# Kernel tuning notes

Hardware: AMD Instinct MI355X
Metric: run time of the kernel (lower is better)

Reference implementation:

```python
import jax, jax.numpy as jnp
import numpy as np

N = 32768      # total nodes (512 graphs x 64 padded nodes)
E = 262144     # edges (avg degree 8)
F_IN = 74      # atom feature dim
D0 = 128       # dim_embedding
D1 = 256       # hidden feats
B = 512        # batch_size (graphs)
NPG = 64       # nodes per graph
EPS = 1e-5     # BatchNorm1d eps


def setup_inputs() -> dict:
    key = jax.random.key(0)
    ks = jax.random.split(key, 8)
    def rn(k, shape, s=0.05):
        return jax.random.normal(k, shape, jnp.float32) * s
    # init_transform weight [D0, F_IN]; padding=True zeroes the last row
    W_init = rn(ks[0], (D0, F_IN)).at[-1].set(0.0)
    return {
        "node_feats": jax.random.normal(ks[1], (N, F_IN), jnp.float32),
        "W_init": W_init,
        "gcn_w1": rn(ks[2], (D0, D1)), "gcn_b1": jnp.zeros((D1,), jnp.float32),
        "res_w1": rn(ks[3], (D1, D0)), "res_b1": jnp.zeros((D1,), jnp.float32),
        "bn_g1": jnp.ones((D1,), jnp.float32), "bn_b1": jnp.zeros((D1,), jnp.float32),
        "gcn_w2": rn(ks[4], (D1, D1)), "gcn_b2": jnp.zeros((D1,), jnp.float32),
        "bn_g2": jnp.ones((D1,), jnp.float32), "bn_b2": jnp.zeros((D1,), jnp.float32),
        "edge_src": jax.random.randint(ks[5], (E,), 0, N),
        "edge_dst": jax.random.randint(ks[6], (E,), 0, N),
    }


def _agg(x, src, dst):
    # DGL GraphConv norm='both': D_out^{-1/2} gather-scatter D_in^{-1/2}, degrees clamped to >= 1
    ones = jnp.ones((src.shape[0],), x.dtype)
    deg_out = jnp.clip(jax.ops.segment_sum(ones, src, num_segments=N), 1.0)
    deg_in = jnp.clip(jax.ops.segment_sum(ones, dst, num_segments=N), 1.0)
    xs = x * jax.lax.rsqrt(deg_out)[:, None]
    agg = jax.ops.segment_sum(xs[src], dst, num_segments=N)  # [N, d]
    return agg * jax.lax.rsqrt(deg_in)[:, None]


def _bn(x, g, b):
    # BatchNorm1d training-mode: batch stats over node axis, biased var
    m = x.mean(0)
    v = x.var(0)
    return (x - m) * jax.lax.rsqrt(v + EPS) * g + b


def reference(node_feats, W_init, gcn_w1, gcn_b1, res_w1, res_b1, bn_g1, bn_b1,
              gcn_w2, gcn_b2, bn_g2, bn_b2, edge_src, edge_dst):
    h = node_feats @ W_init.T  # [N, D0]
    # layer 1: residual Linear 128->256, GCN(aggregate then weight, since in<out), GELU, BN
    res = h @ res_w1.T + res_b1
    g = jax.nn.gelu(_agg(h, edge_src, edge_dst) @ gcn_w1 + gcn_b1, approximate=False)
    h = _bn(g + res, bn_g1, bn_b1)
    # layer 2: Identity residual
    g = jax.nn.gelu(_agg(h, edge_src, edge_dst) @ gcn_w2 + gcn_b2, approximate=False)
    h = _bn(g + h, bn_g2, bn_b2)
    return h.reshape(B, NPG, D1)
```

## Files before the change

kernel.cpp:

```cpp
#include <hip/hip_runtime.h>
#include <hip/hip_bf16.h>
#include <math.h>

#define N_NODES 32768
#define E_EDGES 262144
#define F_INF   74
#define KP      96
#define D0      128
#define D1      256
#define BN_EPS  1e-5f
#define RBLK    1024

typedef float f32x4 __attribute__((ext_vector_type(4)));
typedef short s16x8 __attribute__((ext_vector_type(8)));

__device__ __forceinline__ float b2f(ushort h) { return __uint_as_float(((unsigned)h) << 16); }
__device__ __forceinline__ ushort f2b(float f) {
    unsigned u = __float_as_uint(f);
    return (ushort)((u + 0x7FFFu + ((u >> 16) & 1u)) >> 16);
}
__device__ __forceinline__ float gelu_exact(float x) {
    return 0.5f * x * (1.0f + erff(x * 0.70710678118654752440f));
}


__global__ void k_degrees(const int* __restrict__ src, const int* __restrict__ dst,
                          int* __restrict__ deg) {
    int e = blockIdx.x * 256 + threadIdx.x;
    if (e < E_EDGES) {
        atomicAdd(&deg[src[e]], 1);
        atomicAdd(&deg[N_NODES + dst[e]], 1);
    }
}

__global__ __launch_bounds__(1024) void k_scan(const int* __restrict__ deg,
                                               int* __restrict__ row_off,
                                               float* __restrict__ rsq_out,
                                               float* __restrict__ rsq_in,
                                               int* __restrict__ cursor) {
    __shared__ int part[1024];
    int t = threadIdx.x;
    int base = t * 32;
    int loc[32];
    int s = 0;
    #pragma unroll
    for (int i = 0; i < 32; i++) { loc[i] = s; s += deg[N_NODES + base + i]; }
    part[t] = s;
    #pragma unroll
    for (int i = 0; i < 32; i++) {
        int n = base + i;
        int d_o = deg[n];           if (d_o < 1) d_o = 1;
        int d_i = deg[N_NODES + n]; if (d_i < 1) d_i = 1;
        rsq_out[n] = 1.0f / sqrtf((float)d_o);
        rsq_in[n]  = 1.0f / sqrtf((float)d_i);
        cursor[n] = 0;
    }
    __syncthreads();
    for (int off = 1; off < 1024; off <<= 1) {
        int v = 0;
        if (t >= off) v = part[t - off];
        __syncthreads();
        if (t >= off) part[t] += v;
        __syncthreads();
    }
    int pre = (t == 0) ? 0 : part[t - 1];
    #pragma unroll
    for (int i = 0; i < 32; i++) row_off[base + i] = pre + loc[i];
    if (t == 1023) row_off[N_NODES] = part[1023];
}

__global__ void k_fill(const int* __restrict__ src, const int* __restrict__ dst,
                       const int* __restrict__ row_off, const float* __restrict__ rsq_out,
                       int* __restrict__ cursor, int* __restrict__ csr_src,
                       float* __restrict__ esc) {
    int e = blockIdx.x * 256 + threadIdx.x;
    if (e < E_EDGES) {
        int d = dst[e];
        int s = src[e];
        int slot = atomicAdd(&cursor[d], 1);
        int pos = row_off[d] + slot;
        csr_src[pos] = s;
        esc[pos] = rsq_out[s];
    }
}


__global__ void k_prep(const float* __restrict__ nf, const float* __restrict__ Wi,
                       const float* __restrict__ w1, const float* __restrict__ rw,
                       const float* __restrict__ w2,
                       ushort* __restrict__ nfB, ushort* __restrict__ WTB,
                       ushort* __restrict__ WB1, ushort* __restrict__ RWB,
                       ushort* __restrict__ WB2) {
    int idx = blockIdx.x * 256 + threadIdx.x;
    {
        int n = idx / KP, k = idx - n * KP;
        nfB[idx] = (k < F_INF) ? f2b(nf[n * F_INF + k]) : (ushort)0;
    }
    if (idx < D0 * KP) {
        int c = idx / KP, k = idx - c * KP;
        WTB[idx] = (k < F_INF) ? f2b(Wi[c * F_INF + k]) : (ushort)0;
    }
    if (idx < D1 * D0) {
        int n = idx >> 7, k = idx & 127;
        WB1[idx] = f2b(w1[k * D1 + n]);
        RWB[idx] = f2b(rw[idx]);
    }
    if (idx < D1 * D1) {
        int n = idx >> 8, k = idx & 255;
        WB2[idx] = f2b(w2[k * D1 + n]);
    }
}


__global__ __launch_bounds__(512) void k_init_mfma(
    const ushort* __restrict__ nfB, const ushort* __restrict__ WTB,
    ushort* __restrict__ h0) {
    int tid = threadIdx.x;
    int w = tid >> 6, lane = tid & 63, m = lane & 15, g4 = lane >> 4;
    int col = w * 16 + m;
    int rbase = blockIdx.x * 16;
    s16x8 B[3], A[3];
    #pragma unroll
    for (int j = 0; j < 3; j++)
        B[j] = *reinterpret_cast<const s16x8*>(&WTB[(size_t)col * KP + j * 32 + g4 * 8]);
    #pragma unroll
    for (int j = 0; j < 3; j++)
        A[j] = *reinterpret_cast<const s16x8*>(&nfB[(size_t)(rbase + m) * KP + j * 32 + g4 * 8]);
    f32x4 acc = (f32x4){0.f, 0.f, 0.f, 0.f};
    #pragma unroll
    for (int j = 0; j < 3; j++)
        acc = __builtin_amdgcn_mfma_f32_16x16x32_bf16(A[j], B[j], acc, 0, 0, 0);
    #pragma unroll
    for (int r = 0; r < 4; r++)
        h0[(size_t)(rbase + g4 * 4 + r) * D0 + col] = f2b(acc[r]);
}


__global__ __launch_bounds__(512) void k_layer1f(
    const ushort* __restrict__ h0B, const float* __restrict__ rsq_in,
    const int* __restrict__ row_off, const int* __restrict__ csr_src,
    const float* __restrict__ esc,
    const ushort* __restrict__ WB1, const ushort* __restrict__ RWB,
    const float* __restrict__ b1, const float* __restrict__ rb,
    ushort* __restrict__ t1B, float* __restrict__ partials) {
    __shared__ ushort sA[32 * 128];
    int tid = threadIdx.x;
    int rbase = blockIdx.x * 32;
    {
        int nloc = tid >> 4;
        int node = rbase + nloc;
        int f = (tid & 15) * 8;
        int beg = row_off[node], end = row_off[node + 1];
        float a[8];
        #pragma unroll
        for (int j = 0; j < 8; j++) a[j] = 0.f;
        int e = beg;
        for (; e + 3 < end; e += 4) {
            int s0 = csr_src[e], s1 = csr_src[e + 1], s2 = csr_src[e + 2], s3 = csr_src[e + 3];
            float c0 = esc[e], c1 = esc[e + 1], c2 = esc[e + 2], c3 = esc[e + 3];
            s16x8 v0 = *reinterpret_cast<const s16x8*>(&h0B[(size_t)s0 * D0 + f]);
            s16x8 v1 = *reinterpret_cast<const s16x8*>(&h0B[(size_t)s1 * D0 + f]);
            s16x8 v2 = *reinterpret_cast<const s16x8*>(&h0B[(size_t)s2 * D0 + f]);
            s16x8 v3 = *reinterpret_cast<const s16x8*>(&h0B[(size_t)s3 * D0 + f]);
            #pragma unroll
            for (int j = 0; j < 8; j++)
                a[j] += b2f((ushort)v0[j]) * c0 + b2f((ushort)v1[j]) * c1 +
                        b2f((ushort)v2[j]) * c2 + b2f((ushort)v3[j]) * c3;
        }
        for (; e < end; e++) {
            int s = csr_src[e];
            float sc = esc[e];
            s16x8 v = *reinterpret_cast<const s16x8*>(&h0B[(size_t)s * D0 + f]);
            #pragma unroll
            for (int j = 0; j < 8; j++) a[j] += b2f((ushort)v[j]) * sc;
        }
        float si = rsq_in[node];
        s16x8 o;
        #pragma unroll
        for (int j = 0; j < 8; j++) o[j] = (short)f2b(a[j] * si);
        int boff = nloc * 256 + ((f * 2) ^ ((nloc & 15) << 4));
        *reinterpret_cast<s16x8*>(((char*)sA) + boff) = o;
    }
    __syncthreads();
    int w = tid >> 6, lane = tid & 63, m = lane & 15, g4 = lane >> 4;
    int cb = w * 32;
    s16x8 BG[2][4], BR[2][4];
    #pragma unroll
    for (int nt = 0; nt < 2; nt++)
        #pragma unroll
        for (int j = 0; j < 4; j++) {
            BG[nt][j] = *reinterpret_cast<const s16x8*>(&WB1[(size_t)(cb + nt * 16 + m) * D0 + j * 32 + g4 * 8]);
            BR[nt][j] = *reinterpret_cast<const s16x8*>(&RWB[(size_t)(cb + nt * 16 + m) * D0 + j * 32 + g4 * 8]);
        }
    float bg[2], brv[2];
    #pragma unroll
    for (int nt = 0; nt < 2; nt++) {
        bg[nt]  = b1[cb + nt * 16 + m];
        brv[nt] = rb[cb + nt * 16 + m];
    }
    float ps[2] = {0.f, 0.f}, pq[2] = {0.f, 0.f};
    #pragma unroll
    for (int rt = 0; rt < 2; rt++) {
        int row = rt * 16 + m;
        s16x8 aA[4], aH[4];
        #pragma unroll
        for (int j = 0; j < 4; j++) {
            int boff = row * 256 + (((j * 4 + g4) * 16) ^ ((row & 15) << 4));
            aA[j] = *reinterpret_cast<const s16x8*>(((const char*)sA) + boff);
            aH[j] = *reinterpret_cast<const s16x8*>(&h0B[(size_t)(rbase + row) * D0 + j * 32 + g4 * 8]);
        }
        f32x4 accG[2], accR[2];
        #pragma unroll
        for (int nt = 0; nt < 2; nt++) {
            accG[nt] = (f32x4){0.f, 0.f, 0.f, 0.f};
            accR[nt] = (f32x4){0.f, 0.f, 0.f, 0.f};
        }
        #pragma unroll
        for (int j = 0; j < 4; j++)
            #pragma unroll
            for (int nt = 0; nt < 2; nt++) {
                accG[nt] = __builtin_amdgcn_mfma_f32_16x16x32_bf16(aA[j], BG[nt][j], accG[nt], 0, 0, 0);
                accR[nt] = __builtin_amdgcn_mfma_f32_16x16x32_bf16(aH[j], BR[nt][j], accR[nt], 0, 0, 0);
            }
        #pragma unroll
        for (int nt = 0; nt < 2; nt++) {
            int col = cb + nt * 16 + m;
            #pragma unroll
            for (int r = 0; r < 4; r++) {
                int orow = rbase + rt * 16 + g4 * 4 + r;
                float v = gelu_exact(accG[nt][r] + bg[nt]) + accR[nt][r] + brv[nt];
                t1B[(size_t)orow * D1 + col] = f2b(v);
                ps[nt] += v; pq[nt] += v * v;
            }
        }
    }
    #pragma unroll
    for (int nt = 0; nt < 2; nt++) {
        float s = ps[nt], q = pq[nt];
        s += __shfl_xor(s, 16); s += __shfl_xor(s, 32);
        q += __shfl_xor(q, 16); q += __shfl_xor(q, 32);
        if (g4 == 0) {
            int col = cb + nt * 16 + m;
            partials[(size_t)col * RBLK + blockIdx.x] = s;
            partials[(size_t)(256 + col) * RBLK + blockIdx.x] = q;
        }
    }
}


__global__ __launch_bounds__(512) void k_layer2f(
    const ushort* __restrict__ t1B,
    const float* __restrict__ sc1, const float* __restrict__ sh1,
    const float* __restrict__ rsq_in,
    const int* __restrict__ row_off, const int* __restrict__ csr_src,
    const float* __restrict__ esc,
    const ushort* __restrict__ WB2, const float* __restrict__ b2,
    ushort* __restrict__ t2B, float* __restrict__ partials) {
    __shared__ ushort sA[32 * 256];
    int tid = threadIdx.x;
    int rbase = blockIdx.x * 32;
    {
        int nloc = tid >> 4;
        int node = rbase + nloc;
        int f0 = (tid & 15) * 8;
        int beg = row_off[node], end = row_off[node + 1];
        float a0[8], a1[8];
        #pragma unroll
        for (int j = 0; j < 8; j++) { a0[j] = 0.f; a1[j] = 0.f; }
        float ssum = 0.f;
        int e = beg;
        for (; e + 1 < end; e += 2) {
            int s0 = csr_src[e], s1 = csr_src[e + 1];
            float c0 = esc[e], c1 = esc[e + 1];
            s16x8 v00 = *reinterpret_cast<const s16x8*>(&t1B[(size_t)s0 * D1 + f0]);
            s16x8 v01 = *reinterpret_cast<const s16x8*>(&t1B[(size_t)s0 * D1 + f0 + 128]);
            s16x8 v10 = *reinterpret_cast<const s16x8*>(&t1B[(size_t)s1 * D1 + f0]);
            s16x8 v11 = *reinterpret_cast<const s16x8*>(&t1B[(size_t)s1 * D1 + f0 + 128]);
            ssum += c0 + c1;
            #pragma unroll
            for (int j = 0; j < 8; j++) {
                a0[j] += b2f((ushort)v00[j]) * c0 + b2f((ushort)v10[j]) * c1;
                a1[j] += b2f((ushort)v01[j]) * c0 + b2f((ushort)v11[j]) * c1;
            }
        }
        for (; e < end; e++) {
            int s = csr_src[e];
            float sc = esc[e];
            s16x8 v0 = *reinterpret_cast<const s16x8*>(&t1B[(size_t)s * D1 + f0]);
            s16x8 v1 = *reinterpret_cast<const s16x8*>(&t1B[(size_t)s * D1 + f0 + 128]);
            ssum += sc;
            #pragma unroll
            for (int j = 0; j < 8; j++) {
                a0[j] += b2f((ushort)v0[j]) * sc;
                a1[j] += b2f((ushort)v1[j]) * sc;
            }
        }
        float si = rsq_in[node];
        s16x8 o0, o1;
        #pragma unroll
        for (int j = 0; j < 8; j++) {
            o0[j] = (short)f2b((sc1[f0 + j] * a0[j] + sh1[f0 + j] * ssum) * si);
            o1[j] = (short)f2b((sc1[f0 + 128 + j] * a1[j] + sh1[f0 + 128 + j] * ssum) * si);
        }
        int swz = (nloc & 15) << 4;
        int b0 = nloc * 512 + ((f0 * 2) ^ swz);
        int b1_ = nloc * 512 + (((f0 + 128) * 2) ^ swz);
        *reinterpret_cast<s16x8*>(((char*)sA) + b0) = o0;
        *reinterpret_cast<s16x8*>(((char*)sA) + b1_) = o1;
    }
    __syncthreads();
    int w = tid >> 6, lane = tid & 63, m = lane & 15, g4 = lane >> 4;
    int cb = w * 32;
    ushort rres[2][2][4];
    #pragma unroll
    for (int nt = 0; nt < 2; nt++) {
        int col = cb + nt * 16 + m;
        #pragma unroll
        for (int rt = 0; rt < 2; rt++)
            #pragma unroll
            for (int r = 0; r < 4; r++)
                rres[nt][rt][r] = t1B[(size_t)(rbase + rt * 16 + g4 * 4 + r) * D1 + col];
    }
    s16x8 BG[2][8];
    #pragma unroll
    for (int nt = 0; nt < 2; nt++)
        #pragma unroll
        for (int j = 0; j < 8; j++)
            BG[nt][j] = *reinterpret_cast<const s16x8*>(&WB2[(size_t)(cb + nt * 16 + m) * D1 + j * 32 + g4 * 8]);
    float bg[2], a1c[2], s1c[2];
    #pragma unroll
    for (int nt = 0; nt < 2; nt++) {
        int col = cb + nt * 16 + m;
        bg[nt] = b2[col]; a1c[nt] = sc1[col]; s1c[nt] = sh1[col];
    }
    float ps[2] = {0.f, 0.f}, pq[2] = {0.f, 0.f};
    #pragma unroll
    for (int rt = 0; rt < 2; rt++) {
        int row = rt * 16 + m;
        s16x8 aA[8];
        #pragma unroll
        for (int j = 0; j < 8; j++) {
            int boff = row * 512 + (((j * 4 + g4) * 16) ^ ((row & 15) << 4));
            aA[j] = *reinterpret_cast<const s16x8*>(((const char*)sA) + boff);
        }
        f32x4 acc[2];
        #pragma unroll
        for (int nt = 0; nt < 2; nt++) acc[nt] = (f32x4){0.f, 0.f, 0.f, 0.f};
        #pragma unroll
        for (int j = 0; j < 8; j++)
            #pragma unroll
            for (int nt = 0; nt < 2; nt++)
                acc[nt] = __builtin_amdgcn_mfma_f32_16x16x32_bf16(aA[j], BG[nt][j], acc[nt], 0, 0, 0);
        #pragma unroll
        for (int nt = 0; nt < 2; nt++) {
            int col = cb + nt * 16 + m;
            #pragma unroll
            for (int r = 0; r < 4; r++) {
                int orow = rbase + rt * 16 + g4 * 4 + r;
                float h1v = fmaf(b2f(rres[nt][rt][r]), a1c[nt], s1c[nt]);
                float v = gelu_exact(acc[nt][r] + bg[nt]) + h1v;
                t2B[(size_t)orow * D1 + col] = f2b(v);
                ps[nt] += v; pq[nt] += v * v;
            }
        }
    }
    #pragma unroll
    for (int nt = 0; nt < 2; nt++) {
        float s = ps[nt], q = pq[nt];
        s += __shfl_xor(s, 16); s += __shfl_xor(s, 32);
        q += __shfl_xor(q, 16); q += __shfl_xor(q, 32);
        if (g4 == 0) {
            int col = cb + nt * 16 + m;
            partials[(size_t)col * RBLK + blockIdx.x] = s;
            partials[(size_t)(256 + col) * RBLK + blockIdx.x] = q;
        }
    }
}


__global__ __launch_bounds__(256) void k_reduce(
    const float* __restrict__ partials, const float* __restrict__ g,
    const float* __restrict__ b, float* __restrict__ sc, float* __restrict__ sh) {
    int c = blockIdx.x;
    int t = threadIdx.x;
    const float* ps = partials + (size_t)c * RBLK;
    const float* pq = partials + (size_t)(256 + c) * RBLK;
    float s = ps[t] + ps[t + 256] + ps[t + 512] + ps[t + 768];
    float q = pq[t] + pq[t + 256] + pq[t + 512] + pq[t + 768];
    __shared__ float Ls[256], Lq[256];
    Ls[t] = s; Lq[t] = q;
    __syncthreads();
    for (int o = 128; o > 0; o >>= 1) {
        if (t < o) { Ls[t] += Ls[t + o]; Lq[t] += Lq[t + o]; }
        __syncthreads();
    }
    if (t == 0) {
        float m = Ls[0] * (1.0f / (float)N_NODES);
        float var = Lq[0] * (1.0f / (float)N_NODES) - m * m;
        float a = g[c] / sqrtf(var + BN_EPS);
        sc[c] = a;
        sh[c] = b[c] - m * a;
    }
}


__global__ __launch_bounds__(256) void k_apply(
    const ushort* __restrict__ t2B, const float* __restrict__ sc,
    const float* __restrict__ sh, float* __restrict__ out) {
    int idx = blockIdx.x * 256 + threadIdx.x;
    size_t base = (size_t)idx * 8;
    int c = (int)(base & 255);
    s16x8 v = *reinterpret_cast<const s16x8*>(&t2B[base]);
    float4 o0, o1;
    o0.x = fmaf(b2f((ushort)v[0]), sc[c + 0], sh[c + 0]);
    o0.y = fmaf(b2f((ushort)v[1]), sc[c + 1], sh[c + 1]);
    o0.z = fmaf(b2f((ushort)v[2]), sc[c + 2], sh[c + 2]);
    o0.w = fmaf(b2f((ushort)v[3]), sc[c + 3], sh[c + 3]);
    o1.x = fmaf(b2f((ushort)v[4]), sc[c + 4], sh[c + 4]);
    o1.y = fmaf(b2f((ushort)v[5]), sc[c + 5], sh[c + 5]);
    o1.z = fmaf(b2f((ushort)v[6]), sc[c + 6], sh[c + 6]);
    o1.w = fmaf(b2f((ushort)v[7]), sc[c + 7], sh[c + 7]);
    *reinterpret_cast<float4*>(&out[base]) = o0;
    *reinterpret_cast<float4*>(&out[base + 4]) = o1;
}


static inline size_t align256(size_t x) { return (x + 255) & ~(size_t)255; }

extern "C" void kernel_launch(void* const* d_in, const int* in_sizes, int n_in,
                              void* d_out, int out_size, void* d_ws, size_t ws_size,
                              hipStream_t stream) {
    const float* node_feats = (const float*)d_in[0];
    const float* W_init     = (const float*)d_in[1];
    const float* gcn_w1     = (const float*)d_in[2];
    const float* gcn_b1     = (const float*)d_in[3];
    const float* res_w1     = (const float*)d_in[4];
    const float* res_b1     = (const float*)d_in[5];
    const float* bn_g1      = (const float*)d_in[6];
    const float* bn_b1      = (const float*)d_in[7];
    const float* gcn_w2     = (const float*)d_in[8];
    const float* gcn_b2     = (const float*)d_in[9];
    const float* bn_g2      = (const float*)d_in[10];
    const float* bn_b2      = (const float*)d_in[11];
    const int*   edge_src   = (const int*)d_in[12];
    const int*   edge_dst   = (const int*)d_in[13];
    float* out = (float*)d_out;

    char* p = (char*)d_ws;
    size_t off = 0;
    auto take = [&](size_t bytes) { void* r = p + off; off += align256(bytes); return r; };

    ushort* h0B   = (ushort*)take((size_t)N_NODES * D0 * 2);
    ushort* t1B   = (ushort*)take((size_t)N_NODES * D1 * 2);
    ushort* t2B   = (ushort*)take((size_t)N_NODES * D1 * 2);
    ushort* nfB   = (ushort*)take((size_t)N_NODES * KP * 2);
    ushort* WTB   = (ushort*)take((size_t)D0 * KP * 2);
    ushort* WB1   = (ushort*)take((size_t)D1 * D0 * 2);
    ushort* RWB   = (ushort*)take((size_t)D1 * D0 * 2);
    ushort* WB2   = (ushort*)take((size_t)D1 * D1 * 2);
    float*  part1 = (float*)take((size_t)2 * 256 * RBLK * 4);
    float*  part2 = (float*)take((size_t)2 * 256 * RBLK * 4);
    float*  sc1   = (float*)take(256 * 4);
    float*  sh1   = (float*)take(256 * 4);
    float*  sc2   = (float*)take(256 * 4);
    float*  sh2   = (float*)take(256 * 4);
    float*  rsq_out = (float*)take((size_t)N_NODES * 4);
    float*  rsq_in  = (float*)take((size_t)N_NODES * 4);
    int*    degi    = (int*)take((size_t)2 * N_NODES * 4);
    int*    cursor  = (int*)take((size_t)N_NODES * 4);
    int*    row_off = (int*)take((size_t)(N_NODES + 2) * 4);
    int*    csr_src = (int*)take((size_t)E_EDGES * 4);
    float*  esc     = (float*)take((size_t)E_EDGES * 4);

    hipMemsetAsync(degi, 0, (size_t)2 * N_NODES * 4, stream);

    k_degrees<<<(E_EDGES + 255) / 256, 256, 0, stream>>>(edge_src, edge_dst, degi);
    k_scan<<<1, 1024, 0, stream>>>(degi, row_off, rsq_out, rsq_in, cursor);
    k_fill<<<(E_EDGES + 255) / 256, 256, 0, stream>>>(edge_src, edge_dst, row_off, rsq_out,
                                                      cursor, csr_src, esc);

    k_prep<<<(N_NODES * KP) / 256, 256, 0, stream>>>(node_feats, W_init, gcn_w1, res_w1, gcn_w2,
                                                     nfB, WTB, WB1, RWB, WB2);

    k_init_mfma<<<N_NODES / 16, 512, 0, stream>>>(nfB, WTB, h0B);

    k_layer1f<<<RBLK, 512, 0, stream>>>(h0B, rsq_in, row_off, csr_src, esc,
                                        WB1, RWB, gcn_b1, res_b1, t1B, part1);
    k_reduce<<<256, 256, 0, stream>>>(part1, bn_g1, bn_b1, sc1, sh1);

    k_layer2f<<<RBLK, 512, 0, stream>>>(t1B, sc1, sh1, rsq_in, row_off, csr_src, esc,
                                        WB2, gcn_b2, t2B, part2);
    k_reduce<<<256, 256, 0, stream>>>(part2, bn_g2, bn_b2, sc2, sh2);

    k_apply<<<(N_NODES * D1 / 8) / 256, 256, 0, stream>>>(t2B, sc2, sh2, out);
}
```

Measured before the change: 219.1 us.

## Merge front-end kernels by block-range dispatch and unroll layer-2 gather by four

Merges the degree-count and weight/feature conversion kernels into one launch, and the CSR fill and the initial MFMA projection into another, routing each block to its task by block index. This cuts the launch count from five to three and lets independent work run concurrently. The layer-2 neighbor gather loop is also unrolled from two to four edges per iteration to keep more loads in flight. The cost is higher register pressure in layer 2, plus mixed block types sharing the GPU within each fused launch.

```diff
diff --git a/kernel.cpp b/kernel.cpp
--- a/kernel.cpp
+++ b/kernel.cpp
@@ -24,12 +24,39 @@
 }
 
 
-__global__ void k_degrees(const int* __restrict__ src, const int* __restrict__ dst,
-                          int* __restrict__ deg) {
-    int e = blockIdx.x * 256 + threadIdx.x;
-    if (e < E_EDGES) {
+__global__ void k_front_a(const int* __restrict__ src, const int* __restrict__ dst,
+                          int* __restrict__ deg,
+                          const float* __restrict__ nf, const float* __restrict__ Wi,
+                          const float* __restrict__ w1, const float* __restrict__ rw,
+                          const float* __restrict__ w2,
+                          ushort* __restrict__ nfB, ushort* __restrict__ WTB,
+                          ushort* __restrict__ WB1, ushort* __restrict__ RWB,
+                          ushort* __restrict__ WB2) {
+    int bid = blockIdx.x;
+    int tid = threadIdx.x;
+    if (bid < 1024) {
+        int e = bid * 256 + tid;
         atomicAdd(&deg[src[e]], 1);
         atomicAdd(&deg[N_NODES + dst[e]], 1);
+        return;
+    }
+    int idx = (bid - 1024) * 256 + tid;
+    {
+        int n = idx / KP, k = idx - n * KP;
+        nfB[idx] = (k < F_INF) ? f2b(nf[n * F_INF + k]) : (ushort)0;
+    }
+    if (idx < D0 * KP) {
+        int c = idx / KP, k = idx - c * KP;
+        WTB[idx] = (k < F_INF) ? f2b(Wi[c * F_INF + k]) : (ushort)0;
+    }
+    if (idx < D1 * D0) {
+        int n = idx >> 7, k = idx & 127;
+        WB1[idx] = f2b(w1[k * D1 + n]);
+        RWB[idx] = f2b(rw[idx]);
+    }
+    if (idx < D1 * D1) {
+        int n = idx >> 8, k = idx & 255;
+        WB2[idx] = f2b(w2[k * D1 + n]);
     }
 }
 
@@ -69,56 +96,29 @@
     if (t == 1023) row_off[N_NODES] = part[1023];
 }
 
-__global__ void k_fill(const int* __restrict__ src, const int* __restrict__ dst,
-                       const int* __restrict__ row_off, const float* __restrict__ rsq_out,
-                       int* __restrict__ cursor, int* __restrict__ csr_src,
-                       float* __restrict__ esc) {
-    int e = blockIdx.x * 256 + threadIdx.x;
-    if (e < E_EDGES) {
+
+__global__ __launch_bounds__(512) void k_front_b(
+    const int* __restrict__ src, const int* __restrict__ dst,
+    const int* __restrict__ row_off, const float* __restrict__ rsq_out,
+    int* __restrict__ cursor, int* __restrict__ csr_src, float* __restrict__ esc,
+    const ushort* __restrict__ nfB, const ushort* __restrict__ WTB,
+    ushort* __restrict__ h0) {
+    int bid = blockIdx.x;
+    int tid = threadIdx.x;
+    if (bid < 512) {
+        int e = bid * 512 + tid;
         int d = dst[e];
         int s = src[e];
         int slot = atomicAdd(&cursor[d], 1);
         int pos = row_off[d] + slot;
         csr_src[pos] = s;
         esc[pos] = rsq_out[s];
-    }
-}
-
-
-__global__ void k_prep(const float* __restrict__ nf, const float* __restrict__ Wi,
-                       const float* __restrict__ w1, const float* __restrict__ rw,
-                       const float* __restrict__ w2,
-                       ushort* __restrict__ nfB, ushort* __restrict__ WTB,
-                       ushort* __restrict__ WB1, ushort* __restrict__ RWB,
-                       ushort* __restrict__ WB2) {
-    int idx = blockIdx.x * 256 + threadIdx.x;
-    {
-        int n = idx / KP, k = idx - n * KP;
-        nfB[idx] = (k < F_INF) ? f2b(nf[n * F_INF + k]) : (ushort)0;
-    }
-    if (idx < D0 * KP) {
-        int c = idx / KP, k = idx - c * KP;
-        WTB[idx] = (k < F_INF) ? f2b(Wi[c * F_INF + k]) : (ushort)0;
-    }
-    if (idx < D1 * D0) {
-        int n = idx >> 7, k = idx & 127;
-        WB1[idx] = f2b(w1[k * D1 + n]);
-        RWB[idx] = f2b(rw[idx]);
-    }
-    if (idx < D1 * D1) {
-        int n = idx >> 8, k = idx & 255;
-        WB2[idx] = f2b(w2[k * D1 + n]);
-    }
-}
-
-
-__global__ __launch_bounds__(512) void k_init_mfma(
-    const ushort* __restrict__ nfB, const ushort* __restrict__ WTB,
-    ushort* __restrict__ h0) {
-    int tid = threadIdx.x;
+        return;
+    }
+    int b2 = bid - 512;
     int w = tid >> 6, lane = tid & 63, m = lane & 15, g4 = lane >> 4;
     int col = w * 16 + m;
-    int rbase = blockIdx.x * 16;
+    int rbase = b2 * 16;
     s16x8 B[3], A[3];
     #pragma unroll
     for (int j = 0; j < 3; j++)
@@ -269,25 +269,31 @@
         for (int j = 0; j < 8; j++) { a0[j] = 0.f; a1[j] = 0.f; }
         float ssum = 0.f;
         int e = beg;
-        for (; e + 1 < end; e += 2) {
-            int s0 = csr_src[e], s1 = csr_src[e + 1];
-            float c0 = esc[e], c1 = esc[e + 1];
-            s16x8 v00 = *reinterpret_cast<const s16x8*>(&t1B[(size_t)s0 * D1 + f0]);
-            s16x8 v01 = *reinterpret_cast<const s16x8*>(&t1B[(size_t)s0 * D1 + f0 + 128]);
-            s16x8 v10 = *reinterpret_cast<const s16x8*>(&t1B[(size_t)s1 * D1 + f0]);
-            s16x8 v11 = *reinterpret_cast<const s16x8*>(&t1B[(size_t)s1 * D1 + f0 + 128]);
-            ssum += c0 + c1;
+        for (; e + 3 < end; e += 4) {
+            int s0 = csr_src[e], s1 = csr_src[e + 1], s2 = csr_src[e + 2], s3 = csr_src[e + 3];
+            float c0 = esc[e], c1 = esc[e + 1], c2 = esc[e + 2], c3 = esc[e + 3];
+            const s16x8* p0 = reinterpret_cast<const s16x8*>(&t1B[(size_t)s0 * D1 + f0]);
+            const s16x8* p1 = reinterpret_cast<const s16x8*>(&t1B[(size_t)s1 * D1 + f0]);
+            const s16x8* p2 = reinterpret_cast<const s16x8*>(&t1B[(size_t)s2 * D1 + f0]);
+            const s16x8* p3 = reinterpret_cast<const s16x8*>(&t1B[(size_t)s3 * D1 + f0]);
+            s16x8 v00 = p0[0], v01 = p0[16];
+            s16x8 v10 = p1[0], v11 = p1[16];
+            s16x8 v20 = p2[0], v21 = p2[16];
+            s16x8 v30 = p3[0], v31 = p3[16];
+            ssum += c0 + c1 + c2 + c3;
             #pragma unroll
             for (int j = 0; j < 8; j++) {
-                a0[j] += b2f((ushort)v00[j]) * c0 + b2f((ushort)v10[j]) * c1;
-                a1[j] += b2f((ushort)v01[j]) * c0 + b2f((ushort)v11[j]) * c1;
+                a0[j] += b2f((ushort)v00[j]) * c0 + b2f((ushort)v10[j]) * c1 +
+                         b2f((ushort)v20[j]) * c2 + b2f((ushort)v30[j]) * c3;
+                a1[j] += b2f((ushort)v01[j]) * c0 + b2f((ushort)v11[j]) * c1 +
+                         b2f((ushort)v21[j]) * c2 + b2f((ushort)v31[j]) * c3;
             }
         }
         for (; e < end; e++) {
             int s = csr_src[e];
             float sc = esc[e];
-            s16x8 v0 = *reinterpret_cast<const s16x8*>(&t1B[(size_t)s * D1 + f0]);
-            s16x8 v1 = *reinterpret_cast<const s16x8*>(&t1B[(size_t)s * D1 + f0 + 128]);
+            const s16x8* p = reinterpret_cast<const s16x8*>(&t1B[(size_t)s * D1 + f0]);
+            s16x8 v0 = p[0], v1 = p[16];
             ssum += sc;
             #pragma unroll
             for (int j = 0; j < 8; j++) {
@@ -474,15 +480,14 @@
 
     hipMemsetAsync(degi, 0, (size_t)2 * N_NODES * 4, stream);
 
-    k_degrees<<<(E_EDGES + 255) / 256, 256, 0, stream>>>(edge_src, edge_dst, degi);
+    k_front_a<<<1024 + (N_NODES * KP) / 256, 256, 0, stream>>>(
+        edge_src, edge_dst, degi, node_feats, W_init, gcn_w1, res_w1, gcn_w2,
+        nfB, WTB, WB1, RWB, WB2);
+
     k_scan<<<1, 1024, 0, stream>>>(degi, row_off, rsq_out, rsq_in, cursor);
-    k_fill<<<(E_EDGES + 255) / 256, 256, 0, stream>>>(edge_src, edge_dst, row_off, rsq_out,
-                                                      cursor, csr_src, esc);
-
-    k_prep<<<(N_NODES * KP) / 256, 256, 0, stream>>>(node_feats, W_init, gcn_w1, res_w1, gcn_w2,
-                                                     nfB, WTB, WB1, RWB, WB2);
-
-    k_init_mfma<<<N_NODES / 16, 512, 0, stream>>>(nfB, WTB, h0B);
+
+    k_front_b<<<512 + N_NODES / 16, 512, 0, stream>>>(
+        edge_src, edge_dst, row_off, rsq_out, cursor, csr_src, esc, nfB, WTB, h0B);
 
     k_layer1f<<<RBLK, 512, 0, stream>>>(h0B, rsq_in, row_off, csr_src, esc,
                                         WB1, RWB, gcn_b1, res_b1, t1B, part1);
```

Result: faster. 211.7 us (-3.4%).
